# Kernel tuning notes

Hardware: AMD Instinct MI355X
Metric: run time of the kernel (lower is better)

## Reference

```python
import math
import jax, jax.numpy as jnp
import numpy as np

B, N, C = 2, 21760, 256
L, Hh, P = 4, 8, 4
Dh = C // Hh


def setup_inputs() -> dict:
    key = jax.random.key(0)
    ks = jax.random.split(key, 8)
    shapes = np.array([[128, 128], [64, 64], [32, 32], [16, 16]], dtype=np.int64)
    areas = shapes[:, 0] * shapes[:, 1]
    start_ids = np.concatenate([[0], np.cumsum(areas)[:-1]]).astype(np.int64)
    S = int(areas.sum())  # 21760

    in_feats = jax.random.normal(ks[0], (B, N, C), jnp.float32)
    sample_priors = jax.random.uniform(ks[1], (B, N, L, 2), jnp.float32)
    sample_feats = jax.random.normal(ks[2], (B, S, C), jnp.float32)

    # sampling_offsets: zero-init weight in torch; use small random so offsets vary,
    # bias is the canonical deformable-DETR grid init.
    W_off = jax.random.normal(ks[3], (C, Hh * L * P * 2), jnp.float32) * 0.01
    thetas = jnp.arange(Hh, dtype=jnp.float32) * (2.0 * math.pi / Hh)
    grid = jnp.stack([jnp.cos(thetas), jnp.sin(thetas)], axis=1)  # [Hh,2]
    grid = grid / jnp.max(jnp.abs(grid), axis=1, keepdims=True)
    grid = jnp.tile(grid[:, None, None, :], (1, L, P, 1))  # [Hh,L,P,2]
    sizes = jnp.arange(1, P + 1, dtype=jnp.float32).reshape(1, 1, P, 1)
    b_off = (sizes * grid).reshape(-1)  # [Hh*L*P*2]

    W_attn = jax.random.normal(ks[4], (C, Hh * L * P), jnp.float32) * 0.01
    b_attn = jnp.zeros((Hh * L * P,), jnp.float32)
    W_val = jax.random.normal(ks[5], (C, C), jnp.float32) / math.sqrt(C)
    b_val = jnp.zeros((C,), jnp.float32)
    W_out = jax.random.normal(ks[6], (C, C), jnp.float32) / math.sqrt(C)
    b_out = jnp.zeros((C,), jnp.float32)

    return dict(in_feats=in_feats, sample_priors=sample_priors, sample_feats=sample_feats,
                sample_map_shapes=jnp.asarray(shapes), sample_map_start_ids=jnp.asarray(start_ids),
                W_off=W_off, b_off=b_off, W_attn=W_attn, b_attn=b_attn,
                W_val=W_val, b_val=b_val, W_out=W_out, b_out=b_out)


def _msda_core(value, shapes_np, starts_np, loc, attn_w):
    """value: [B,S,Hh,Dh]; loc: [B,N,Hh,L,P,2] in [0,1]; attn_w: [B,N,Hh,L,P].
    Bilinear sampling matching grid_sample(align_corners=False, padding='zeros')."""
    b, n = loc.shape[:2]
    acc = jnp.zeros((b, n, Hh, Dh), value.dtype)
    for l in range(L):
        H_l, W_l = int(shapes_np[l, 0]), int(shapes_np[l, 1])
        s0 = int(starts_np[l])
        v = value[:, s0:s0 + H_l * W_l]  # [B,S_l,Hh,Dh]
        lx = loc[:, :, :, l, :, 0] * W_l - 0.5  # [B,N,Hh,P] pixel coords
        ly = loc[:, :, :, l, :, 1] * H_l - 0.5
        x0f, y0f = jnp.floor(lx), jnp.floor(ly)
        wx1, wy1 = lx - x0f, ly - y0f
        wx0, wy0 = 1.0 - wx1, 1.0 - wy1
        x0, y0 = x0f.astype(jnp.int32), y0f.astype(jnp.int32)

        def gather(xi, yi):
            valid = ((xi >= 0) & (xi < W_l) & (yi >= 0) & (yi < H_l)).astype(v.dtype)
            idx = jnp.clip(yi, 0, H_l - 1) * W_l + jnp.clip(xi, 0, W_l - 1)  # [B,N,Hh,P]
            idx_t = idx.transpose(0, 1, 3, 2).reshape(b, n * P, Hh)
            g = jnp.take_along_axis(v, idx_t[..., None], axis=1)  # [B,N*P,Hh,Dh]
            g = g.reshape(b, n, P, Hh, Dh).transpose(0, 1, 3, 2, 4)  # [B,N,Hh,P,Dh]
            return g * valid[..., None]

        samp = (gather(x0, y0) * (wx0 * wy0)[..., None]
                + gather(x0 + 1, y0) * (wx1 * wy0)[..., None]
                + gather(x0, y0 + 1) * (wx0 * wy1)[..., None]
                + gather(x0 + 1, y0 + 1) * (wx1 * wy1)[..., None])
        acc = acc + jnp.einsum('bnhpd,bnhp->bnhd', samp, attn_w[:, :, :, l, :])
    return acc


def reference(in_feats, sample_priors, sample_feats, sample_map_shapes, sample_map_start_ids,
              W_off, b_off, W_attn, b_attn, W_val, b_val, W_out, b_out):
    b, n = in_feats.shape[:2]
    # structural constants (level geometry)
    shapes_np = np.asarray(jax.device_get(sample_map_shapes))
    starts_np = np.asarray(jax.device_get(sample_map_start_ids))

    off = (in_feats @ W_off + b_off).reshape(b, n, Hh, L, P, 2)
    normalizer = jnp.flip(sample_map_shapes, axis=-1).astype(in_feats.dtype)  # [L,2] (W,H)
    loc = sample_priors[:, :, None, :, None, :] + off / normalizer[None, None, None, :, None, :]

    aw = jax.nn.softmax((in_feats @ W_attn + b_attn).reshape(b, n, Hh, L * P), axis=-1)
    aw = aw.reshape(b, n, Hh, L, P)

    value = (sample_feats @ W_val + b_val).reshape(b, -1, Hh, Dh)
    weighted = _msda_core(value, shapes_np, starts_np, loc, aw)  # [B,N,Hh,Dh]
    out = weighted.reshape(b, n, Hh * Dh) @ W_out + b_out
    return out
```

## Files before the change

### kernel.cpp

```cpp
#include <hip/hip_runtime.h>
#include <cstdint>

constexpr int kB = 2;
constexpr int kN = 21760;
constexpr int kC = 256;
constexpr int kH = 8;
constexpr int kS = 21760;
constexpr int kM = kB * kN;
constexpr int kMT = 340;

typedef __attribute__((ext_vector_type(8))) short bf16x8;
typedef __attribute__((ext_vector_type(4))) float f32x4;
typedef __attribute__((ext_vector_type(8))) unsigned short us8;

__device__ __forceinline__ float bf2f(unsigned short u) {
  return __uint_as_float(((unsigned int)u) << 16);
}
__device__ __forceinline__ unsigned short f2bf(float f) {
  unsigned int u = __float_as_uint(f);
  u += 0x7fffu + ((u >> 16) & 1u);
  return (unsigned short)(u >> 16);
}
__device__ __forceinline__ float blo(unsigned int v) { return __uint_as_float(v << 16); }
__device__ __forceinline__ float bhi(unsigned int v) { return __uint_as_float(v & 0xffff0000u); }
__device__ __forceinline__ unsigned int cvt_pk_bf16(float lo, float hi) {
  unsigned int r;
  asm("v_cvt_pk_bf16_f32 %0, %1, %2" : "=v"(r) : "v"(lo), "v"(hi));
  return r;
}
__device__ __forceinline__ void gld_lds16(const unsigned short* g, unsigned short* l) {
  __builtin_amdgcn_global_load_lds(
      (const __attribute__((address_space(1))) unsigned int*)g,
      (__attribute__((address_space(3))) unsigned int*)l, 16, 0, 0);
}

__global__ __launch_bounds__(256) void convprep(
    const float* __restrict__ a, const float* __restrict__ b,
    unsigned short* __restrict__ da, unsigned short* __restrict__ db,
    const float* __restrict__ Woff, const float* __restrict__ Wattn,
    const float* __restrict__ Wval, const float* __restrict__ Wout,
    unsigned short* __restrict__ BtOff, unsigned short* __restrict__ BtAttn,
    unsigned short* __restrict__ BtVal, unsigned short* __restrict__ BtOut)
{
  const int bid = blockIdx.x;
  if (bid < 10880) {
    const int tid = bid * 256 + threadIdx.x;
    const int half = kM * 32;
    const float* src; unsigned short* dst; int id;
    if (tid < half) { src = a; dst = da; id = tid; }
    else            { src = b; dst = db; id = tid - half; }
    const int m = id >> 5;
    const int kb = (id & 31) * 8;
    const float4 x0 = *(const float4*)&src[(size_t)m * 256 + kb];
    const float4 x1 = *(const float4*)&src[(size_t)m * 256 + kb + 4];
    us8 o;
    o[0] = f2bf(x0.x); o[1] = f2bf(x0.y); o[2] = f2bf(x0.z); o[3] = f2bf(x0.w);
    o[4] = f2bf(x1.x); o[5] = f2bf(x1.y); o[6] = f2bf(x1.z); o[7] = f2bf(x1.w);
    *(us8*)&dst[(size_t)m * 256 + (kb ^ ((m & 7) << 3))] = o;
  } else {
    const int tid = (bid - 10880) * 256 + threadIdx.x;
    const int r = tid >> 5;
    const int kb = (tid & 31) * 8;
    const float* W; unsigned short* Bt; int n, Nn;
    if (r < 256)      { W = Woff;  Bt = BtOff;  n = r;       Nn = 256; }
    else if (r < 384) { W = Wattn; Bt = BtAttn; n = r - 256; Nn = 128; }
    else if (r < 640) { W = Wval;  Bt = BtVal;  n = r - 384; Nn = 256; }
    else              { W = Wout;  Bt = BtOut;  n = r - 640; Nn = 256; }
    us8 o;
#pragma unroll
    for (int i = 0; i < 8; ++i) o[i] = f2bf(W[(size_t)(kb + i) * Nn + n]);
    *(us8*)&Bt[(size_t)n * 256 + (kb ^ ((n & 7) << 3))] = o;
  }
}

__device__ __forceinline__ void mfma_tile_256(
    const unsigned short* __restrict__ A, const unsigned short* __restrict__ Bt,
    int m0, int n0, int t, unsigned short* As, unsigned short* Bs,
    f32x4 (&acc)[4][4])
{
  const int w = t >> 6, l = t & 63;
  const int wm = w >> 1, wn = w & 1;
  const int srow = l >> 3;
  const int skb  = (l & 7) * 8;

  for (int kt = 0; kt < 256; kt += 64) {
#pragma unroll
    for (int i = 0; i < 4; ++i) {
      const int c = i * 4 + w;
      const int row = c * 8 + srow;
      gld_lds16(A + (size_t)(m0 + row) * 256 + kt + skb, &As[c * 512]);
    }
#pragma unroll
    for (int i = 0; i < 4; ++i) {
      const int c = i * 4 + w;
      const int row = c * 8 + srow;
      gld_lds16(Bt + (size_t)(n0 + row) * 256 + kt + skb, &Bs[c * 512]);
    }
    __syncthreads();

#pragma unroll
    for (int s = 0; s < 2; ++s) {
      bf16x8 afr[4], bfr[4];
      const int kf = s * 32 + ((l >> 4) * 8);
#pragma unroll
      for (int i = 0; i < 4; ++i) {
        const int row = wm * 64 + i * 16 + (l & 15);
        afr[i] = *(const bf16x8*)&As[row * 64 + (kf ^ ((row & 7) << 3))];
      }
#pragma unroll
      for (int j = 0; j < 4; ++j) {
        const int col = wn * 64 + j * 16 + (l & 15);
        bfr[j] = *(const bf16x8*)&Bs[col * 64 + (kf ^ ((col & 7) << 3))];
      }
#pragma unroll
      for (int i = 0; i < 4; ++i)
#pragma unroll
        for (int j = 0; j < 4; ++j)
          acc[i][j] = __builtin_amdgcn_mfma_f32_16x16x32_bf16(afr[i], bfr[j], acc[i][j], 0, 0, 0);
    }
    __syncthreads();
  }
}

__global__ __launch_bounds__(256) void gemm_lead(
    const unsigned short* __restrict__ in_bf,
    const unsigned short* __restrict__ s_bf,
    const unsigned short* __restrict__ BtOA,
    const unsigned short* __restrict__ BtVal,
    const float* __restrict__ b_off, const float* __restrict__ b_attn,
    const float* __restrict__ b_val,
    unsigned short* __restrict__ off_hm,
    unsigned short* __restrict__ attn_hm,
    unsigned short* __restrict__ val_hm)
{
  const int bid = blockIdx.x;
  const int x = bid & 7;
  const int slot = bid >> 3;
  int mode, nt, mh;
  if (slot < 129) { mode = 0; nt = slot % 3; mh = slot / 3; }
  else            { mode = 1; const int s2 = slot - 129; nt = s2 % 2; mh = s2 / 2; }
  const int m = mh * 8 + x;
  if (m >= kMT) return;
  const int m0 = m * 128, n0 = nt * 128;

  __shared__ unsigned short As[128 * 64];
  __shared__ unsigned short Bs[128 * 64];
  const int t = threadIdx.x;

  f32x4 acc[4][4] = {};
  mfma_tile_256(mode ? s_bf : in_bf, mode ? BtVal : BtOA, m0, n0, t, As, Bs, acc);

  const int w = t >> 6, l = t & 63;
  const int wm = w >> 1, wn = w & 1;
  const int lr = l >> 4;
#pragma unroll
  for (int j = 0; j < 4; ++j) {
    const int col = n0 + wn * 64 + j * 16 + (l & 15);
    const float bv = mode ? b_val[col] : (col < 256 ? b_off[col] : b_attn[col - 256]);
#pragma unroll
    for (int i = 0; i < 4; ++i) {
      const int rbase = m0 + wm * 64 + i * 16 + lr * 4;
#pragma unroll
      for (int r = 0; r < 4; ++r) {
        const float v = acc[i][j][r] + bv;
        const int row = rbase + r;
        if (mode == 1) {
          const int bb = row >= kS;
          const int s2 = row - bb * kS;
          val_hm[((size_t)(bb * 8 + (col >> 5)) * kS + s2) * 32 + (col & 31)] = f2bf(v);
        } else if (col < 256) {
          off_hm[((size_t)(col >> 5) * kM + row) * 32 + (col & 31)] = f2bf(v);
        } else {
          const int c2 = col - 256;
          attn_hm[((size_t)(c2 >> 4) * kM + row) * 16 + (c2 & 15)] = f2bf(v);
        }
      }
    }
  }
}

__global__ __launch_bounds__(256) void gemm_out(
    const unsigned short* __restrict__ wgt,
    const unsigned short* __restrict__ BtOut,
    const float* __restrict__ b_out,
    float* __restrict__ out)
{
  const int bid = blockIdx.x;
  const int x = bid & 7;
  const int slot = bid >> 3;
  const int nt = slot % 2;
  const int mh = slot / 2;
  const int m = mh * 8 + x;
  if (m >= kMT) return;
  const int m0 = m * 128, n0 = nt * 128;

  __shared__ unsigned short As[128 * 64];
  __shared__ unsigned short Bs[128 * 64];
  const int t = threadIdx.x;

  f32x4 acc[4][4] = {};
  mfma_tile_256(wgt, BtOut, m0, n0, t, As, Bs, acc);

  const int w = t >> 6, l = t & 63;
  const int wm = w >> 1, wn = w & 1;
  const int lr = l >> 4;
#pragma unroll
  for (int j = 0; j < 4; ++j) {
    const int col = n0 + wn * 64 + j * 16 + (l & 15);
    const float bv = b_out[col];
#pragma unroll
    for (int i = 0; i < 4; ++i) {
      const int rbase = m0 + wm * 64 + i * 16 + lr * 4;
#pragma unroll
      for (int r = 0; r < 4; ++r)
        out[(size_t)(rbase + r) * 256 + col] = acc[i][j][r] + bv;
    }
  }
}

__global__ __launch_bounds__(256, 4) void msda_kernel(
    const unsigned short* __restrict__ off_hm,
    const unsigned short* __restrict__ attn_hm,
    const unsigned short* __restrict__ val_bf,
    const float* __restrict__ priors,
    unsigned short* __restrict__ wgt)
{
  __shared__ int s_rec[16 * 136];
  const int bid = blockIdx.x;
  const int plane = bid & 15;
  const int chunk = bid >> 4;
  const int b = plane >> 3, h = plane & 7;
  const int t = threadIdx.x;
  const int ql = t >> 4;
  const int q = b * kN + chunk * 16 + ql;

  {
    const int j = t & 15;
    const int lv = j >> 2;

    const float lgt = bf2f(attn_hm[((size_t)h * kM + q) * 16 + j]);
    float mx = lgt;
#pragma unroll
    for (int m = 8; m; m >>= 1) mx = fmaxf(mx, __shfl_xor(mx, m, 16));
    const float p = __expf(lgt - mx);
    float sum = p;
#pragma unroll
    for (int m = 8; m; m >>= 1) sum += __shfl_xor(sum, m, 16);
    const float wN = p / sum;

    const unsigned int oo = *(const unsigned int*)&off_hm[((size_t)h * kM + q) * 32 + j * 2];
    const float ox = blo(oo);
    const float oy = bhi(oo);
    const float2 pr = *(const float2*)&priors[(size_t)q * 8 + lv * 2];

    const int Wl = 128 >> lv;
    const float fW = (float)Wl;
    const float lx = fmaf(pr.x, fW, ox) - 0.5f;
    const float ly = fmaf(pr.y, fW, oy) - 0.5f;
    const float x0f = floorf(lx), y0f = floorf(ly);
    const float wx1 = lx - x0f, wy1 = ly - y0f;
    const float wx0 = 1.f - wx1, wy0 = 1.f - wy1;
    const int x0 = (int)x0f, y0 = (int)y0f;
    const int start = (int)((0x5400500040000000ull >> (16 * lv)) & 0xffff);

    const bool vx0 = (x0 >= 0) & (x0 < Wl);
    const bool vx1 = (x0 + 1 >= 0) & (x0 + 1 < Wl);
    const bool vy0 = (y0 >= 0) & (y0 < Wl);
    const bool vy1 = (y0 + 1 >= 0) & (y0 + 1 < Wl);
    const int xc0 = min(max(x0, 0), Wl - 1);
    const int xc1 = min(max(x0 + 1, 0), Wl - 1);
    const int yc0 = min(max(y0, 0), Wl - 1);
    const int yc1 = min(max(y0 + 1, 0), Wl - 1);

    const int rt = start + yc0 * Wl;
    const int rb = start + yc1 * Wl;

    int4 r0, r1;
    r0.x = (rt + xc0) * 64; r0.y = __float_as_int((vx0 & vy0) ? wN * wx0 * wy0 : 0.f);
    r0.z = (rt + xc1) * 64; r0.w = __float_as_int((vx1 & vy0) ? wN * wx1 * wy0 : 0.f);
    r1.x = (rb + xc0) * 64; r1.y = __float_as_int((vx0 & vy1) ? wN * wx0 * wy1 : 0.f);
    r1.z = (rb + xc1) * 64; r1.w = __float_as_int((vx1 & vy1) ? wN * wx1 * wy1 : 0.f);

    const int base = ql * 136 + j * 8;
    *(int4*)&s_rec[base] = r0;
    *(int4*)&s_rec[base + 4] = r1;
  }
  __syncthreads();

  const int lane = t & 15;
  const int c = lane >> 2;
  const int k = lane & 3;
  const char* plane_base = (const char*)val_bf + (size_t)plane * kS * 64 + k * 16;
  const int* rp = &s_rec[ql * 136 + c * 2];

  float a0 = 0.f, a1 = 0.f, a2 = 0.f, a3 = 0.f;
  float a4 = 0.f, a5 = 0.f, a6 = 0.f, a7 = 0.f;
#pragma unroll
  for (int B = 0; B < 2; ++B) {
    int2 r[8];
#pragma unroll
    for (int j = 0; j < 8; ++j) r[j] = *(const int2*)&rp[(B * 8 + j) * 8];
    uint4 v[8];
#pragma unroll
    for (int j = 0; j < 8; ++j) v[j] = *(const uint4*)(plane_base + r[j].x);
#pragma unroll
    for (int j = 0; j < 8; ++j) {
      const float w = __int_as_float(r[j].y);
      a0 = fmaf(w, blo(v[j].x), a0); a1 = fmaf(w, bhi(v[j].x), a1);
      a2 = fmaf(w, blo(v[j].y), a2); a3 = fmaf(w, bhi(v[j].y), a3);
      a4 = fmaf(w, blo(v[j].z), a4); a5 = fmaf(w, bhi(v[j].z), a5);
      a6 = fmaf(w, blo(v[j].w), a6); a7 = fmaf(w, bhi(v[j].w), a7);
    }
  }

#pragma unroll
  for (int m = 4; m <= 8; m <<= 1) {
    a0 += __shfl_xor(a0, m); a1 += __shfl_xor(a1, m);
    a2 += __shfl_xor(a2, m); a3 += __shfl_xor(a3, m);
    a4 += __shfl_xor(a4, m); a5 += __shfl_xor(a5, m);
    a6 += __shfl_xor(a6, m); a7 += __shfl_xor(a7, m);
  }

  if (c == 0) {
    const int c0 = h * 32 + k * 8;
    const int dst = c0 ^ ((q & 7) << 3);
    uint4 o;
    o.x = cvt_pk_bf16(a0, a1);
    o.y = cvt_pk_bf16(a2, a3);
    o.z = cvt_pk_bf16(a4, a5);
    o.w = cvt_pk_bf16(a6, a7);
    *(uint4*)&wgt[(size_t)q * 256 + dst] = o;
  }
}

extern "C" void kernel_launch(void* const* d_in, const int* in_sizes, int n_in,
                              void* d_out, int out_size, void* d_ws, size_t ws_size,
                              hipStream_t stream) {
  const float* in_feats = (const float*)d_in[0];
  const float* priors   = (const float*)d_in[1];
  const float* sfeats   = (const float*)d_in[2];
  const float* W_off  = (const float*)d_in[5];
  const float* b_off  = (const float*)d_in[6];
  const float* W_attn = (const float*)d_in[7];
  const float* b_attn = (const float*)d_in[8];
  const float* W_val  = (const float*)d_in[9];
  const float* b_val  = (const float*)d_in[10];
  const float* W_out  = (const float*)d_in[11];
  const float* b_out  = (const float*)d_in[12];
  float* out = (float*)d_out;

  unsigned short* in_bf   = (unsigned short*)d_ws;
  unsigned short* s_bf    = in_bf   + (size_t)kM * 256;
  unsigned short* off_hm  = s_bf    + (size_t)kM * 256;
  unsigned short* attn_hm = off_hm  + (size_t)kM * 256;
  unsigned short* val_hm  = attn_hm + (size_t)kM * 128;
  unsigned short* wgt_bf  = val_hm  + (size_t)kM * 256;
  unsigned short* BtOff   = wgt_bf  + (size_t)kM * 256;
  unsigned short* BtAttn  = BtOff   + 256 * 256;
  unsigned short* BtVal   = BtAttn  + 128 * 256;
  unsigned short* BtOut   = BtVal   + 256 * 256;

  const dim3 blk(256);

  convprep<<<dim3(10992), blk, 0, stream>>>(
      in_feats, sfeats, in_bf, s_bf,
      W_off, W_attn, W_val, W_out, BtOff, BtAttn, BtVal, BtOut);

  gemm_lead<<<dim3(8 * 215), blk, 0, stream>>>(
      in_bf, s_bf, BtOff, BtVal, b_off, b_attn, b_val, off_hm, attn_hm, val_hm);

  msda_kernel<<<dim3(kM / 2), blk, 0, stream>>>(off_hm, attn_hm, val_hm, priors, wgt_bf);

  gemm_out<<<dim3(8 * 2 * 43), blk, 0, stream>>>(wgt_bf, BtOut, b_out, out);
}
```

Before: 145.8 us.

## Fuse fp32-to-bf16 activation conversion into lead GEMM with full-K A tile in LDS

Removes the separate conversion pass that wrote bf16 copies of in_feats and sample_feats to workspace. Each gemm_lead block now loads its 128-row fp32 A tile once, converts it to bf16 into a 64KB LDS buffer covering all of K, and loops over every N tile so A is reused. This drops a full read and write of both activation tensors. In exchange there are fewer, larger-LDS blocks (680), which lowers occupancy, and the in-block N loop is serial.

```diff
diff --git a/kernel.cpp b/kernel.cpp
--- a/kernel.cpp
+++ b/kernel.cpp
@@ -34,42 +34,132 @@
       (__attribute__((address_space(3))) unsigned int*)l, 16, 0, 0);
 }
 
-__global__ __launch_bounds__(256) void convprep(
-    const float* __restrict__ a, const float* __restrict__ b,
-    unsigned short* __restrict__ da, unsigned short* __restrict__ db,
+__global__ __launch_bounds__(256) void prep_weights(
     const float* __restrict__ Woff, const float* __restrict__ Wattn,
     const float* __restrict__ Wval, const float* __restrict__ Wout,
     unsigned short* __restrict__ BtOff, unsigned short* __restrict__ BtAttn,
     unsigned short* __restrict__ BtVal, unsigned short* __restrict__ BtOut)
 {
+  const int tid = blockIdx.x * 256 + threadIdx.x;
+  const int r = tid >> 5;
+  const int kb = (tid & 31) * 8;
+  const float* W; unsigned short* Bt; int n, Nn;
+  if (r < 256)      { W = Woff;  Bt = BtOff;  n = r;       Nn = 256; }
+  else if (r < 384) { W = Wattn; Bt = BtAttn; n = r - 256; Nn = 128; }
+  else if (r < 640) { W = Wval;  Bt = BtVal;  n = r - 384; Nn = 256; }
+  else              { W = Wout;  Bt = BtOut;  n = r - 640; Nn = 256; }
+  us8 o;
+#pragma unroll
+  for (int i = 0; i < 8; ++i) o[i] = f2bf(W[(size_t)(kb + i) * Nn + n]);
+  *(us8*)&Bt[(size_t)n * 256 + (kb ^ ((n & 7) << 3))] = o;
+}
+
+__global__ __launch_bounds__(256) void gemm_lead(
+    const float* __restrict__ in_feats,
+    const float* __restrict__ sfeats,
+    const unsigned short* __restrict__ BtOA,
+    const unsigned short* __restrict__ BtVal,
+    const float* __restrict__ b_off, const float* __restrict__ b_attn,
+    const float* __restrict__ b_val,
+    unsigned short* __restrict__ off_hm,
+    unsigned short* __restrict__ attn_hm,
+    unsigned short* __restrict__ val_hm)
+{
+  __shared__ unsigned short Afull[4 * 128 * 64];
+  __shared__ unsigned short Bs[128 * 64];
+
   const int bid = blockIdx.x;
-  if (bid < 10880) {
-    const int tid = bid * 256 + threadIdx.x;
-    const int half = kM * 32;
-    const float* src; unsigned short* dst; int id;
-    if (tid < half) { src = a; dst = da; id = tid; }
-    else            { src = b; dst = db; id = tid - half; }
-    const int m = id >> 5;
-    const int kb = (id & 31) * 8;
-    const float4 x0 = *(const float4*)&src[(size_t)m * 256 + kb];
-    const float4 x1 = *(const float4*)&src[(size_t)m * 256 + kb + 4];
-    us8 o;
-    o[0] = f2bf(x0.x); o[1] = f2bf(x0.y); o[2] = f2bf(x0.z); o[3] = f2bf(x0.w);
-    o[4] = f2bf(x1.x); o[5] = f2bf(x1.y); o[6] = f2bf(x1.z); o[7] = f2bf(x1.w);
-    *(us8*)&dst[(size_t)m * 256 + (kb ^ ((m & 7) << 3))] = o;
-  } else {
-    const int tid = (bid - 10880) * 256 + threadIdx.x;
-    const int r = tid >> 5;
-    const int kb = (tid & 31) * 8;
-    const float* W; unsigned short* Bt; int n, Nn;
-    if (r < 256)      { W = Woff;  Bt = BtOff;  n = r;       Nn = 256; }
-    else if (r < 384) { W = Wattn; Bt = BtAttn; n = r - 256; Nn = 128; }
-    else if (r < 640) { W = Wval;  Bt = BtVal;  n = r - 384; Nn = 256; }
-    else              { W = Wout;  Bt = BtOut;  n = r - 640; Nn = 256; }
-    us8 o;
-#pragma unroll
-    for (int i = 0; i < 8; ++i) o[i] = f2bf(W[(size_t)(kb + i) * Nn + n]);
-    *(us8*)&Bt[(size_t)n * 256 + (kb ^ ((n & 7) << 3))] = o;
+  const int mode = (bid >= kMT) ? 1 : 0;
+  const int m = mode ? (bid - kMT) : bid;
+  const int m0 = m * 128;
+  const int NT = mode ? 2 : 3;
+  const unsigned short* Bt = mode ? BtVal : BtOA;
+
+  const int t = threadIdx.x;
+  const int w = t >> 6, l = t & 63;
+  const int wm = w >> 1, wn = w & 1;
+
+  {
+    const int arow = t >> 1;
+    const int khalf = (t & 1) * 128;
+    const float* Af = (mode ? sfeats : in_feats) + (size_t)(m0 + arow) * 256 + khalf;
+    const int swz = (arow & 7) << 3;
+#pragma unroll
+    for (int i = 0; i < 32; ++i) {
+      const int col = khalf + i * 4;
+      const float4 f = *(const float4*)&Af[i * 4];
+      uint2 o;
+      o.x = cvt_pk_bf16(f.x, f.y);
+      o.y = cvt_pk_bf16(f.z, f.w);
+      *(uint2*)&Afull[(col >> 6) * 8192 + arow * 64 + ((col & 63) ^ swz)] = o;
+    }
+  }
+
+  const int srow = l >> 3;
+  const int skb  = (l & 7) * 8;
+  const int lr = l >> 4;
+
+  for (int nt = 0; nt < NT; ++nt) {
+    const int n0 = nt * 128;
+    f32x4 acc[4][4] = {};
+
+    for (int kt = 0; kt < 256; kt += 64) {
+#pragma unroll
+      for (int i = 0; i < 4; ++i) {
+        const int c = i * 4 + w;
+        const int row = c * 8 + srow;
+        gld_lds16(Bt + (size_t)(n0 + row) * 256 + kt + skb, &Bs[c * 512]);
+      }
+      __syncthreads();
+
+      const int kc = kt >> 6;
+#pragma unroll
+      for (int s = 0; s < 2; ++s) {
+        bf16x8 afr[4], bfr[4];
+        const int kf = s * 32 + ((l >> 4) * 8);
+#pragma unroll
+        for (int i = 0; i < 4; ++i) {
+          const int row = wm * 64 + i * 16 + (l & 15);
+          afr[i] = *(const bf16x8*)&Afull[kc * 8192 + row * 64 + (kf ^ ((row & 7) << 3))];
+        }
+#pragma unroll
+        for (int j = 0; j < 4; ++j) {
+          const int col = wn * 64 + j * 16 + (l & 15);
+          bfr[j] = *(const bf16x8*)&Bs[col * 64 + (kf ^ ((col & 7) << 3))];
+        }
+#pragma unroll
+        for (int i = 0; i < 4; ++i)
+#pragma unroll
+          for (int j = 0; j < 4; ++j)
+            acc[i][j] = __builtin_amdgcn_mfma_f32_16x16x32_bf16(afr[i], bfr[j], acc[i][j], 0, 0, 0);
+      }
+      __syncthreads();
+    }
+
+#pragma unroll
+    for (int j = 0; j < 4; ++j) {
+      const int col = n0 + wn * 64 + j * 16 + (l & 15);
+      const float bv = mode ? b_val[col] : (col < 256 ? b_off[col] : b_attn[col - 256]);
+#pragma unroll
+      for (int i = 0; i < 4; ++i) {
+        const int rbase = m0 + wm * 64 + i * 16 + lr * 4;
+#pragma unroll
+        for (int r = 0; r < 4; ++r) {
+          const float v = acc[i][j][r] + bv;
+          const int row = rbase + r;
+          if (mode == 1) {
+            const int bb = row >= kS;
+            const int s2 = row - bb * kS;
+            val_hm[((size_t)(bb * 8 + (col >> 5)) * kS + s2) * 32 + (col & 31)] = f2bf(v);
+          } else if (col < 256) {
+            off_hm[((size_t)(col >> 5) * kM + row) * 32 + (col & 31)] = f2bf(v);
+          } else {
+            const int c2 = col - 256;
+            attn_hm[((size_t)(c2 >> 4) * kM + row) * 16 + (c2 & 15)] = f2bf(v);
+          }
+        }
+      }
+    }
   }
 }
 
@@ -119,63 +209,6 @@
           acc[i][j] = __builtin_amdgcn_mfma_f32_16x16x32_bf16(afr[i], bfr[j], acc[i][j], 0, 0, 0);
     }
     __syncthreads();
-  }
-}
-
-__global__ __launch_bounds__(256) void gemm_lead(
-    const unsigned short* __restrict__ in_bf,
-    const unsigned short* __restrict__ s_bf,
-    const unsigned short* __restrict__ BtOA,
-    const unsigned short* __restrict__ BtVal,
-    const float* __restrict__ b_off, const float* __restrict__ b_attn,
-    const float* __restrict__ b_val,
-    unsigned short* __restrict__ off_hm,
-    unsigned short* __restrict__ attn_hm,
-    unsigned short* __restrict__ val_hm)
-{
-  const int bid = blockIdx.x;
-  const int x = bid & 7;
-  const int slot = bid >> 3;
-  int mode, nt, mh;
-  if (slot < 129) { mode = 0; nt = slot % 3; mh = slot / 3; }
-  else            { mode = 1; const int s2 = slot - 129; nt = s2 % 2; mh = s2 / 2; }
-  const int m = mh * 8 + x;
-  if (m >= kMT) return;
-  const int m0 = m * 128, n0 = nt * 128;
-
-  __shared__ unsigned short As[128 * 64];
-  __shared__ unsigned short Bs[128 * 64];
-  const int t = threadIdx.x;
-
-  f32x4 acc[4][4] = {};
-  mfma_tile_256(mode ? s_bf : in_bf, mode ? BtVal : BtOA, m0, n0, t, As, Bs, acc);
-
-  const int w = t >> 6, l = t & 63;
-  const int wm = w >> 1, wn = w & 1;
-  const int lr = l >> 4;
-#pragma unroll
-  for (int j = 0; j < 4; ++j) {
-    const int col = n0 + wn * 64 + j * 16 + (l & 15);
-    const float bv = mode ? b_val[col] : (col < 256 ? b_off[col] : b_attn[col - 256]);
-#pragma unroll
-    for (int i = 0; i < 4; ++i) {
-      const int rbase = m0 + wm * 64 + i * 16 + lr * 4;
-#pragma unroll
-      for (int r = 0; r < 4; ++r) {
-        const float v = acc[i][j][r] + bv;
-        const int row = rbase + r;
-        if (mode == 1) {
-          const int bb = row >= kS;
-          const int s2 = row - bb * kS;
-          val_hm[((size_t)(bb * 8 + (col >> 5)) * kS + s2) * 32 + (col & 31)] = f2bf(v);
-        } else if (col < 256) {
-          off_hm[((size_t)(col >> 5) * kM + row) * 32 + (col & 31)] = f2bf(v);
-        } else {
-          const int c2 = col - 256;
-          attn_hm[((size_t)(c2 >> 4) * kM + row) * 16 + (c2 & 15)] = f2bf(v);
-        }
-      }
-    }
   }
 }
 
@@ -349,9 +382,7 @@
   const float* b_out  = (const float*)d_in[12];
   float* out = (float*)d_out;
 
-  unsigned short* in_bf   = (unsigned short*)d_ws;
-  unsigned short* s_bf    = in_bf   + (size_t)kM * 256;
-  unsigned short* off_hm  = s_bf    + (size_t)kM * 256;
+  unsigned short* off_hm  = (unsigned short*)d_ws;
   unsigned short* attn_hm = off_hm  + (size_t)kM * 256;
   unsigned short* val_hm  = attn_hm + (size_t)kM * 128;
   unsigned short* wgt_bf  = val_hm  + (size_t)kM * 256;
@@ -362,12 +393,12 @@
 
   const dim3 blk(256);
 
-  convprep<<<dim3(10992), blk, 0, stream>>>(
-      in_feats, sfeats, in_bf, s_bf,
+  prep_weights<<<dim3(112), blk, 0, stream>>>(
       W_off, W_attn, W_val, W_out, BtOff, BtAttn, BtVal, BtOut);
 
-  gemm_lead<<<dim3(8 * 215), blk, 0, stream>>>(
-      in_bf, s_bf, BtOff, BtVal, b_off, b_attn, b_val, off_hm, attn_hm, val_hm);
+  gemm_lead<<<dim3(2 * kMT), blk, 0, stream>>>(
+      in_feats, sfeats, BtOff, BtVal, b_off, b_attn, b_val,
+      off_hm, attn_hm, val_hm);
 
   msda_kernel<<<dim3(kM / 2), blk, 0, stream>>>(off_hm, attn_hm, val_hm, priors, wgt_bf);
 
```

After: 168.4 us. 15.5% more time.
